# Kernel tuning notes

Measured on AMD Instinct MI355X. Metric: run time of the kernel, lower is better.

## Reference

```python
import jax, jax.numpy as jnp
import numpy as np

B, W, F, N = 256, 512, 512, 512


def setup_inputs() -> dict:
    key = jax.random.key(0)
    k1, k2, k3, k4, k5 = jax.random.split(key, 5)
    return {
        "x": jax.random.normal(k1, (B, W, F), dtype=jnp.float32),
        "weight_k": jax.random.normal(k2, (F, N), dtype=jnp.float32),
        "weight_q": jax.random.normal(k3, (F, N), dtype=jnp.float32),
        "weight_v": jax.random.normal(k4, (F, N), dtype=jnp.float32),
        "w": jax.random.normal(k5, (W, 1), dtype=jnp.float32),
    }


def reference(x, weight_k, weight_q, weight_v, w):
    # x: (B, W, F)
    n_outputs = weight_k.shape[-1]
    # Per-word K/V projections (original loops over words; here one batched GEMM)
    K = jnp.einsum("bwf,fn->bwn", x, weight_k)  # (B, W, N)
    V = jnp.einsum("bwf,fn->bwn", x, weight_v)  # (B, W, N)
    # Per-sample query: t = x^T @ w -> (F,), q = t @ weight_q -> (N,)
    t = jnp.einsum("bwf,w->bf", x, w[:, 0])     # (B, F)
    Q = t @ weight_q                              # (B, N)
    # Scores over words, scaled, softmax across the word axis
    scores = jnp.einsum("bn,bwn->bw", Q, K) / jnp.sqrt(jnp.float32(n_outputs))
    weights = jax.nn.softmax(scores, axis=1)      # (B, W)
    # Weighted sum of V over words
    return jnp.einsum("bw,bwn->bn", weights, V)   # (B, N)
```

## Files before the change

kernel.cpp:

```cpp
#include <hip/hip_runtime.h>
#include <math.h>

#define B 256
#define W 512
#define F 512
#define N 512
#define GPART 4
#define WPG (W / GPART)

__global__ __launch_bounds__(512) void tpart_kernel(
    const float* __restrict__ x,
    const float* __restrict__ wvec,
    float* __restrict__ t_part)
{
    const int blk = blockIdx.x;
    const int g   = blk & (GPART - 1);
    const int b   = blk >> 2;
    const int tid = threadIdx.x;
    const int ws  = tid >> 7;
    const int f4  = tid & 127;

    __shared__ float s_w[WPG];
    __shared__ float s_part[4][F];

    if (tid < WPG) s_w[tid] = wvec[g * WPG + tid];
    __syncthreads();

    const float* xb = x + (size_t)b * W * F + (size_t)(g * WPG + ws * 32) * F;
    float4 acc = make_float4(0.f, 0.f, 0.f, 0.f);
#pragma unroll 8
    for (int i = 0; i < 32; ++i) {
        const float4 xv = *(const float4*)(xb + (size_t)i * F + f4 * 4);
        const float  ww = s_w[ws * 32 + i];
        acc.x += xv.x * ww; acc.y += xv.y * ww;
        acc.z += xv.z * ww; acc.w += xv.w * ww;
    }
    *(float4*)&s_part[ws][f4 * 4] = acc;
    __syncthreads();

    const float t = (s_part[0][tid] + s_part[1][tid])
                  + (s_part[2][tid] + s_part[3][tid]);
    t_part[(size_t)blk * F + tid] = t;
}

__global__ __launch_bounds__(512) void qr_kernel(
    const float* __restrict__ t_part,
    const float* __restrict__ Wq,
    const float* __restrict__ Wk,
    float* __restrict__ r_out)
{
    __shared__ float s_t[F];
    __shared__ float s_q[N];
    const int b = blockIdx.x, tid = threadIdx.x;

    float t = 0.f;
#pragma unroll
    for (int g = 0; g < GPART; ++g)
        t += t_part[((size_t)b * GPART + g) * F + tid];
    s_t[tid] = t;
    __syncthreads();

    float q0 = 0.f, q1 = 0.f, q2 = 0.f, q3 = 0.f;
#pragma unroll 4
    for (int f = 0; f < F; f += 4) {
        q0 += s_t[f + 0] * Wq[(size_t)(f + 0) * N + tid];
        q1 += s_t[f + 1] * Wq[(size_t)(f + 1) * N + tid];
        q2 += s_t[f + 2] * Wq[(size_t)(f + 2) * N + tid];
        q3 += s_t[f + 3] * Wq[(size_t)(f + 3) * N + tid];
    }
    s_q[tid] = (q0 + q1) + (q2 + q3);
    __syncthreads();

    const float4* wkrow = (const float4*)(Wk + (size_t)tid * N);
    float r0 = 0.f, r1 = 0.f, r2 = 0.f, r3 = 0.f;
#pragma unroll 8
    for (int n4 = 0; n4 < N / 4; ++n4) {
        const float4 kv = wkrow[n4];
        const float4 qv = *(const float4*)&s_q[n4 * 4];
        r0 += kv.x * qv.x; r1 += kv.y * qv.y;
        r2 += kv.z * qv.z; r3 += kv.w * qv.w;
    }
    r_out[(size_t)b * F + tid] =
        ((r0 + r1) + (r2 + r3)) * 0.04419417382415922f;
}

__global__ __launch_bounds__(512) void attn_kernel(
    const float* __restrict__ x,
    const float* __restrict__ Wv,
    const float* __restrict__ r_in,
    float* __restrict__ out)
{
    const int b    = blockIdx.x;
    const int tid  = threadIdx.x;
    const int lane = tid & 63;
    const int wv   = tid >> 6;

    __shared__ float s_c[8][F];
    __shared__ float s_m[8];
    __shared__ float s_l[8];
    __shared__ float s_cf[F];

    const float* xb = x + (size_t)b * W * F;
    const float* rb = r_in + (size_t)b * F;
    const float4 r0 = *(const float4*)(rb + lane * 4);
    const float4 r1 = *(const float4*)(rb + 256 + lane * 4);

    float m = -INFINITY, l = 0.f;
    float4 c0 = make_float4(0.f, 0.f, 0.f, 0.f);
    float4 c1 = make_float4(0.f, 0.f, 0.f, 0.f);

#pragma unroll 2
    for (int t = 0; t < 8; ++t) {
        const float* row = xb + (size_t)(wv * 64 + t * 8) * F;

        float4 xa0[8], xa1[8];
#pragma unroll
        for (int j = 0; j < 8; ++j) {
            xa0[j] = *(const float4*)(row + (size_t)j * F + lane * 4);
            xa1[j] = *(const float4*)(row + (size_t)j * F + 256 + lane * 4);
        }

        float d[8];
#pragma unroll
        for (int j = 0; j < 8; ++j) {
            d[j] = xa0[j].x * r0.x + xa0[j].y * r0.y
                 + xa0[j].z * r0.z + xa0[j].w * r0.w
                 + xa1[j].x * r1.x + xa1[j].y * r1.y
                 + xa1[j].z * r1.z + xa1[j].w * r1.w;
        }

#pragma unroll
        for (int off = 32; off >= 1; off >>= 1) {
#pragma unroll
            for (int j = 0; j < 8; ++j)
                d[j] += __shfl_xor(d[j], off, 64);
        }

        const float mb = fmaxf(fmaxf(fmaxf(d[0], d[1]), fmaxf(d[2], d[3])),
                               fmaxf(fmaxf(d[4], d[5]), fmaxf(d[6], d[7])));
        const float mn = fmaxf(m, mb);
        const float sc = __expf(m - mn);

        float p[8];
        float ps = 0.f;
#pragma unroll
        for (int j = 0; j < 8; ++j) {
            p[j] = __expf(d[j] - mn);
            ps += p[j];
        }
        l = l * sc + ps;

        float ax = c0.x * sc, ay = c0.y * sc, az = c0.z * sc, aw = c0.w * sc;
#pragma unroll
        for (int j = 0; j < 8; ++j) {
            ax += p[j] * xa0[j].x; ay += p[j] * xa0[j].y;
            az += p[j] * xa0[j].z; aw += p[j] * xa0[j].w;
        }
        c0 = make_float4(ax, ay, az, aw);

        ax = c1.x * sc; ay = c1.y * sc; az = c1.z * sc; aw = c1.w * sc;
#pragma unroll
        for (int j = 0; j < 8; ++j) {
            ax += p[j] * xa1[j].x; ay += p[j] * xa1[j].y;
            az += p[j] * xa1[j].z; aw += p[j] * xa1[j].w;
        }
        c1 = make_float4(ax, ay, az, aw);

        m = mn;
    }

    *(float4*)&s_c[wv][lane * 4]       = c0;
    *(float4*)&s_c[wv][256 + lane * 4] = c1;
    if (lane == 0) { s_m[wv] = m; s_l[wv] = l; }
    __syncthreads();

    float M = -INFINITY;
#pragma unroll
    for (int j = 0; j < 8; ++j) M = fmaxf(M, s_m[j]);
    float L = 0.f;
    float alpha[8];
#pragma unroll
    for (int j = 0; j < 8; ++j) {
        alpha[j] = __expf(s_m[j] - M);
        L += alpha[j] * s_l[j];
    }
    const float invL = 1.f / L;

    float cf = 0.f;
#pragma unroll
    for (int j = 0; j < 8; ++j) cf += alpha[j] * s_c[j][tid];
    s_cf[tid] = cf * invL;
    __syncthreads();

    float o0 = 0.f, o1 = 0.f, o2 = 0.f, o3 = 0.f;
#pragma unroll 4
    for (int f = 0; f < F; f += 4) {
        o0 += s_cf[f + 0] * Wv[(size_t)(f + 0) * N + tid];
        o1 += s_cf[f + 1] * Wv[(size_t)(f + 1) * N + tid];
        o2 += s_cf[f + 2] * Wv[(size_t)(f + 2) * N + tid];
        o3 += s_cf[f + 3] * Wv[(size_t)(f + 3) * N + tid];
    }
    out[(size_t)b * N + tid] = (o0 + o1) + (o2 + o3);
}

extern "C" void kernel_launch(void* const* d_in, const int* in_sizes, int n_in,
                              void* d_out, int out_size, void* d_ws, size_t ws_size,
                              hipStream_t stream)
{
    const float* x    = (const float*)d_in[0];
    const float* Wk   = (const float*)d_in[1];
    const float* Wq   = (const float*)d_in[2];
    const float* Wv   = (const float*)d_in[3];
    const float* wvec = (const float*)d_in[4];
    float* out    = (float*)d_out;
    float* t_part = (float*)d_ws;
    float* r      = t_part + (size_t)B * GPART * F;

    tpart_kernel<<<B * GPART, 512, 0, stream>>>(x, wvec, t_part);
    qr_kernel<<<B, 512, 0, stream>>>(t_part, Wq, Wk, r);
    attn_kernel<<<B, 512, 0, stream>>>(x, Wv, r, out);
}
```

Measured before the change: 464.0 us.

## Fuse t-projection, query/key matvecs and attention into one per-batch kernel

Replaces the three-kernel pipeline with a single kernel per batch row that first reduces x against w, then computes q and r = Wk·q in shared memory, then runs the online-softmax attention pass. This removes two kernel launches and the global workspace round trip, and lets the second pass over the batch's x slab potentially hit in cache. In exchange the t reduction uses only 256 blocks instead of 1024, and each block serialises the Wq/Wk matvec phases before the attention loop.

```diff
diff --git a/kernel.cpp b/kernel.cpp
--- a/kernel.cpp
+++ b/kernel.cpp
@@ -5,89 +5,13 @@
 #define W 512
 #define F 512
 #define N 512
-#define GPART 4
-#define WPG (W / GPART)
-
-__global__ __launch_bounds__(512) void tpart_kernel(
+
+__global__ __launch_bounds__(512) void fused_attn_kernel(
     const float* __restrict__ x,
-    const float* __restrict__ wvec,
-    float* __restrict__ t_part)
-{
-    const int blk = blockIdx.x;
-    const int g   = blk & (GPART - 1);
-    const int b   = blk >> 2;
-    const int tid = threadIdx.x;
-    const int ws  = tid >> 7;
-    const int f4  = tid & 127;
-
-    __shared__ float s_w[WPG];
-    __shared__ float s_part[4][F];
-
-    if (tid < WPG) s_w[tid] = wvec[g * WPG + tid];
-    __syncthreads();
-
-    const float* xb = x + (size_t)b * W * F + (size_t)(g * WPG + ws * 32) * F;
-    float4 acc = make_float4(0.f, 0.f, 0.f, 0.f);
-#pragma unroll 8
-    for (int i = 0; i < 32; ++i) {
-        const float4 xv = *(const float4*)(xb + (size_t)i * F + f4 * 4);
-        const float  ww = s_w[ws * 32 + i];
-        acc.x += xv.x * ww; acc.y += xv.y * ww;
-        acc.z += xv.z * ww; acc.w += xv.w * ww;
-    }
-    *(float4*)&s_part[ws][f4 * 4] = acc;
-    __syncthreads();
-
-    const float t = (s_part[0][tid] + s_part[1][tid])
-                  + (s_part[2][tid] + s_part[3][tid]);
-    t_part[(size_t)blk * F + tid] = t;
-}
-
-__global__ __launch_bounds__(512) void qr_kernel(
-    const float* __restrict__ t_part,
     const float* __restrict__ Wq,
     const float* __restrict__ Wk,
-    float* __restrict__ r_out)
-{
-    __shared__ float s_t[F];
-    __shared__ float s_q[N];
-    const int b = blockIdx.x, tid = threadIdx.x;
-
-    float t = 0.f;
-#pragma unroll
-    for (int g = 0; g < GPART; ++g)
-        t += t_part[((size_t)b * GPART + g) * F + tid];
-    s_t[tid] = t;
-    __syncthreads();
-
-    float q0 = 0.f, q1 = 0.f, q2 = 0.f, q3 = 0.f;
-#pragma unroll 4
-    for (int f = 0; f < F; f += 4) {
-        q0 += s_t[f + 0] * Wq[(size_t)(f + 0) * N + tid];
-        q1 += s_t[f + 1] * Wq[(size_t)(f + 1) * N + tid];
-        q2 += s_t[f + 2] * Wq[(size_t)(f + 2) * N + tid];
-        q3 += s_t[f + 3] * Wq[(size_t)(f + 3) * N + tid];
-    }
-    s_q[tid] = (q0 + q1) + (q2 + q3);
-    __syncthreads();
-
-    const float4* wkrow = (const float4*)(Wk + (size_t)tid * N);
-    float r0 = 0.f, r1 = 0.f, r2 = 0.f, r3 = 0.f;
-#pragma unroll 8
-    for (int n4 = 0; n4 < N / 4; ++n4) {
-        const float4 kv = wkrow[n4];
-        const float4 qv = *(const float4*)&s_q[n4 * 4];
-        r0 += kv.x * qv.x; r1 += kv.y * qv.y;
-        r2 += kv.z * qv.z; r3 += kv.w * qv.w;
-    }
-    r_out[(size_t)b * F + tid] =
-        ((r0 + r1) + (r2 + r3)) * 0.04419417382415922f;
-}
-
-__global__ __launch_bounds__(512) void attn_kernel(
-    const float* __restrict__ x,
     const float* __restrict__ Wv,
-    const float* __restrict__ r_in,
+    const float* __restrict__ wvec,
     float* __restrict__ out)
 {
     const int b    = blockIdx.x;
@@ -95,15 +19,83 @@
     const int lane = tid & 63;
     const int wv   = tid >> 6;
 
+    __shared__ float s_w[W];
     __shared__ float s_c[8][F];
+    __shared__ float s_t[F];
+    __shared__ float s_q[N];
+    __shared__ float s_r[F];
     __shared__ float s_m[8];
     __shared__ float s_l[8];
     __shared__ float s_cf[F];
 
     const float* xb = x + (size_t)b * W * F;
-    const float* rb = r_in + (size_t)b * F;
-    const float4 r0 = *(const float4*)(rb + lane * 4);
-    const float4 r1 = *(const float4*)(rb + 256 + lane * 4);
+
+    s_w[tid] = wvec[tid];
+    __syncthreads();
+
+    {
+        float4 t0 = make_float4(0.f, 0.f, 0.f, 0.f);
+        float4 t1 = make_float4(0.f, 0.f, 0.f, 0.f);
+#pragma unroll 2
+        for (int i = 0; i < 64; i += 4) {
+            const float* row = xb + (size_t)(wv * 64 + i) * F;
+            float4 a0[4], a1[4];
+#pragma unroll
+            for (int j = 0; j < 4; ++j) {
+                a0[j] = *(const float4*)(row + (size_t)j * F + lane * 4);
+                a1[j] = *(const float4*)(row + (size_t)j * F + 256 + lane * 4);
+            }
+#pragma unroll
+            for (int j = 0; j < 4; ++j) {
+                const float ww = s_w[wv * 64 + i + j];
+                t0.x += a0[j].x * ww; t0.y += a0[j].y * ww;
+                t0.z += a0[j].z * ww; t0.w += a0[j].w * ww;
+                t1.x += a1[j].x * ww; t1.y += a1[j].y * ww;
+                t1.z += a1[j].z * ww; t1.w += a1[j].w * ww;
+            }
+        }
+        *(float4*)&s_c[wv][lane * 4]       = t0;
+        *(float4*)&s_c[wv][256 + lane * 4] = t1;
+    }
+    __syncthreads();
+
+    {
+        float t = 0.f;
+#pragma unroll
+        for (int j = 0; j < 8; ++j) t += s_c[j][tid];
+        s_t[tid] = t;
+    }
+    __syncthreads();
+
+    {
+        float q0 = 0.f, q1 = 0.f, q2 = 0.f, q3 = 0.f;
+#pragma unroll 4
+        for (int f = 0; f < F; f += 4) {
+            q0 += s_t[f + 0] * Wq[(size_t)(f + 0) * N + tid];
+            q1 += s_t[f + 1] * Wq[(size_t)(f + 1) * N + tid];
+            q2 += s_t[f + 2] * Wq[(size_t)(f + 2) * N + tid];
+            q3 += s_t[f + 3] * Wq[(size_t)(f + 3) * N + tid];
+        }
+        s_q[tid] = (q0 + q1) + (q2 + q3);
+    }
+    __syncthreads();
+
+    {
+        const float4* wkrow = (const float4*)(Wk + (size_t)tid * N);
+        float r0 = 0.f, r1 = 0.f, r2 = 0.f, r3 = 0.f;
+#pragma unroll 8
+        for (int n4 = 0; n4 < N / 4; ++n4) {
+            const float4 kv = wkrow[n4];
+            const float4 qv = *(const float4*)&s_q[n4 * 4];
+            r0 += kv.x * qv.x; r1 += kv.y * qv.y;
+            r2 += kv.z * qv.z; r3 += kv.w * qv.w;
+        }
+        s_r[tid] = ((r0 + r1) + (r2 + r3)) * 0.04419417382415922f;
+    }
+    __syncthreads();
+
+    const float4 r0 = *(const float4*)&s_r[lane * 4];
+    const float4 r1 = *(const float4*)&s_r[256 + lane * 4];
 
     float m = -INFINITY, l = 0.f;
     float4 c0 = make_float4(0.f, 0.f, 0.f, 0.f);
@@ -169,6 +161,7 @@
         m = mn;
     }
 
+    __syncthreads();
     *(float4*)&s_c[wv][lane * 4]       = c0;
     *(float4*)&s_c[wv][256 + lane * 4] = c1;
     if (lane == 0) { s_m[wv] = m; s_l[wv] = l; }
@@ -212,11 +205,7 @@
     const float* Wq   = (const float*)d_in[2];
     const float* Wv   = (const float*)d_in[3];
     const float* wvec = (const float*)d_in[4];
-    float* out    = (float*)d_out;
-    float* t_part = (float*)d_ws;
-    float* r      = t_part + (size_t)B * GPART * F;
-
-    tpart_kernel<<<B * GPART, 512, 0, stream>>>(x, wvec, t_part);
-    qr_kernel<<<B, 512, 0, stream>>>(t_part, Wq, Wk, r);
-    attn_kernel<<<B, 512, 0, stream>>>(x, Wv, r, out);
+    float* out = (float*)d_out;
+
+    fused_attn_kernel<<<B, 512, 0, stream>>>(x, Wq, Wk, Wv, wvec, out);
 }
```

New measurement: 455.0 us. Within noise of the previous version (-1.9%).
